# Performance work log

Hardware: AMD Instinct MI355X
Metric: run time of the kernel (lower is better)

Reference implementation:

```python
import jax, jax.numpy as jnp
import numpy as np

N, DIM, H, D, S, B = 30000, 256, 8, 64, 32, 8
INNER = H * D


def setup_inputs() -> dict:
    key = jax.random.key(0)
    ks = jax.random.split(key, 16)
    def w(k, shape, fan_in):
        return jax.random.normal(k, shape, dtype=jnp.float32) / np.sqrt(fan_in)
    x = jax.random.normal(ks[0], (N, DIM), dtype=jnp.float32)
    batch = jnp.sort(jax.random.randint(ks[1], (N,), 0, B))
    return {
        'x': x,
        'batch': batch,
        'W_fx': w(ks[2], (DIM, INNER), DIM), 'b_fx': jnp.zeros((INNER,), jnp.float32),
        'W_x': w(ks[3], (DIM, INNER), DIM), 'b_x': jnp.zeros((INNER,), jnp.float32),
        'W_slice': w(ks[4], (D, S), D), 'b_slice': jnp.zeros((S,), jnp.float32),
        'graph_temp': 0.5 * jnp.ones((1, H, 1), jnp.float32),
        'W_q': w(ks[5], (D, D), D), 'W_k': w(ks[6], (D, D), D), 'W_v': w(ks[7], (D, D), D),
        'W_out': w(ks[8], (INNER, DIM), INNER), 'b_out': jnp.zeros((DIM,), jnp.float32),
    }


def reference(x, batch, W_fx, b_fx, W_x, b_x, W_slice, b_slice, graph_temp,
              W_q, W_k, W_v, W_out, b_out):
    n = x.shape[0]
    scale = D ** -0.5
    fx = (x @ W_fx + b_fx).reshape(n, H, D)   # [N,H,D]
    xm = (x @ W_x + b_x).reshape(n, H, D)     # [N,H,D]
    # per-node slice assignment weights, tempered softmax over slices
    logits = (jnp.einsum('nhd,ds->nhs', xm, W_slice) + b_slice) / graph_temp
    w = jax.nn.softmax(logits, axis=-1)       # [N,H,S]
    onehot = jax.nn.one_hot(batch, B, dtype=x.dtype)  # [N,B]
    # scatter-add pooling per graph: slice_norm[b,h,s], slice_token[b,h,s,d]
    slice_norm = jax.ops.segment_sum(w, batch, num_segments=B)  # [B,H,S]
    wb = w[:, None, :, :] * onehot[:, :, None, None]            # [N,B,H,S]
    slice_token = jnp.einsum('nbhs,nhd->bhsd', wb, fx)
    slice_token = slice_token / (slice_norm[..., None] + 1e-5)
    # small attention over slice tokens
    q = jnp.einsum('bhsd,de->bhse', slice_token, W_q)
    k = jnp.einsum('bhsd,de->bhse', slice_token, W_k)
    v = jnp.einsum('bhsd,de->bhse', slice_token, W_v)
    attn = jax.nn.softmax(jnp.einsum('bhsd,bhtd->bhst', q, k) * scale, axis=-1)
    out_tok = jnp.einsum('bhst,bhtd->bhsd', attn, v)            # [B,H,S,D]
    # gather back to nodes with weighted reduction over slices
    tmp = jnp.einsum('nhs,bhsd->nbhd', w, out_tok)              # [N,B,H,D]
    out_x = jnp.einsum('nb,nbhd->nhd', onehot, tmp).reshape(n, INNER)
    return out_x @ W_out + b_out
```

## Files before the change

kernel.cpp:

```cpp
#include <hip/hip_runtime.h>

#define NDIM 256
#define INNER 512
#define NH 8
#define ND 64
#define NS 32
#define NB 8
#define NP 30208

typedef __attribute__((ext_vector_type(8))) short short8;
typedef __attribute__((ext_vector_type(4))) float f32x4;

static __device__ __forceinline__ short f2bf(float f) {
  unsigned u = __float_as_uint(f);
  unsigned r = (u + 0x7fffu + ((u >> 16) & 1u)) >> 16;
  return (short)r;
}
static __device__ __forceinline__ float bf2f(short s) {
  return __uint_as_float(((unsigned)(unsigned short)s) << 16);
}

static __device__ __forceinline__ void gl_lds16(const void* g, void* l) {
  __builtin_amdgcn_global_load_lds(
      (const __attribute__((address_space(1))) unsigned int*)g,
      (__attribute__((address_space(3))) unsigned int*)l, 16, 0, 0);
}

__global__ __launch_bounds__(256) void k_xsplit(
    const float* __restrict__ x, short* __restrict__ Xh, short* __restrict__ Xl,
    int total4)
{
  int id = blockIdx.x * 256 + threadIdx.x;
  if (id >= total4) return;
  float4 v = *(const float4*)&x[(size_t)id * 4];
  short h0 = f2bf(v.x), h1 = f2bf(v.y), h2 = f2bf(v.z), h3 = f2bf(v.w);
  short4 hv = make_short4(h0, h1, h2, h3);
  short4 lv = make_short4(f2bf(v.x - bf2f(h0)), f2bf(v.y - bf2f(h1)),
                          f2bf(v.z - bf2f(h2)), f2bf(v.w - bf2f(h3)));
  *(short4*)&Xh[(size_t)id * 4] = hv;
  *(short4*)&Xl[(size_t)id * 4] = lv;
}

__global__ __launch_bounds__(256) void k_prep(
    const float* __restrict__ Wfx, const float* __restrict__ Wx,
    const float* __restrict__ bx, const float* __restrict__ Wsl,
    const float* __restrict__ bsl,
    short* __restrict__ Bt1h, short* __restrict__ Bt1l,
    float* __restrict__ bcomb, int* __restrict__ seg)
{
  int id = blockIdx.x * 256 + threadIdx.x;
  if (id < 131072) {
    int k = id >> 9, n = id & 511;
    float v = Wfx[k * 512 + n];
    short hi = f2bf(v); short lo = f2bf(v - bf2f(hi));
    Bt1h[n * 256 + k] = hi; Bt1l[n * 256 + k] = lo;
  } else if (id < 196608) {
    int e = id - 131072;
    int c = e & 255, k = e >> 8;
    int h = c >> 5, s = c & 31;
    float acc = 0.f;
    #pragma unroll 8
    for (int d = 0; d < 64; d++) acc += Wx[k * 512 + h * 64 + d] * Wsl[d * 32 + s];
    short hi = f2bf(acc); short lo = f2bf(acc - bf2f(hi));
    Bt1h[(512 + c) * 256 + k] = hi; Bt1l[(512 + c) * 256 + k] = lo;
  } else if (id < 196864) {
    int c = id - 196608;
    int h = c >> 5, s = c & 31;
    float acc = bsl[s];
    #pragma unroll 8
    for (int d = 0; d < 64; d++) acc += bx[h * 64 + d] * Wsl[d * 32 + s];
    bcomb[c] = acc;
  } else if (id < 196880) {
    int v = id - 196864;
    seg[v] = (v == 0) ? 0 : 0x7fffffff;
  }
}

__global__ __launch_bounds__(256) void k_segs(
    const int* __restrict__ batch, int* __restrict__ seg, int N)
{
  int i = blockIdx.x * 256 + threadIdx.x;
  if (i >= N) return;
  int b = batch[i];
  int p = (i == 0) ? -1 : batch[i - 1];
  for (int v = p + 1; v <= b; v++)
    if (v >= 1) atomicMin(&seg[v], i);
  if (i == N - 1)
    for (int v = b + 1; v <= 8; v++) atomicMin(&seg[v], N);
}

__global__ __launch_bounds__(512, 4) void k_fxw(
    const short* __restrict__ Xh, const short* __restrict__ Xl,
    const short* __restrict__ Bt1h, const short* __restrict__ Bt1l,
    const float* __restrict__ bfx, const float* __restrict__ bcomb,
    const float* __restrict__ gtemp,
    short* __restrict__ fxTh, short* __restrict__ fxTl,
    short* __restrict__ wh_out, short* __restrict__ wl_out,
    int N, int ntiles)
{
  __shared__ __align__(16) short smem[32768];

  const int lid = blockIdx.x;
  const int xcd = lid & 7;
  const int idx = lid >> 3;
  const int ct  = idx % 6;
  const int rowt = xcd + 8 * (idx / 6);
  if (rowt >= ntiles) return;
  const int row0 = rowt * 128;
  const int tid = threadIdx.x;
  const int lane = tid & 63, l15 = lane & 15, quad = lane >> 4;
  const int wvi = tid >> 6;
  const int wm = wvi & 1, wn = wvi >> 1;
  const int ctbase = ct * 128;
  const int srow = lane & 15, schunk = lane >> 4;

  f32x4 acc[4][2];
  #pragma unroll
  for (int i = 0; i < 4; i++)
    #pragma unroll
    for (int j = 0; j < 2; j++) acc[i][j] = (f32x4){0.f, 0.f, 0.f, 0.f};

  int gr = row0 + wvi * 16 + srow;
  if (gr > N - 1) gr = N - 1;
  const int br = ctbase + wvi * 16 + srow;
  const size_t abase = (size_t)gr * 256 + schunk * 8;
  const size_t bbase = (size_t)br * 256 + schunk * 8;

#define STAGE(p, kt_) do {                                         \
    short* base_ = &smem[(p) * 16384];                             \
    gl_lds16(Xh + abase + (kt_) * 32, base_ + wvi * 512);          \
    gl_lds16(Xl + abase + (kt_) * 32, base_ + 4096 + wvi * 512);   \
    gl_lds16(Bt1h + bbase + (kt_) * 32, base_ + 8192 + wvi * 512); \
    gl_lds16(Bt1l + bbase + (kt_) * 32, base_ + 12288 + wvi * 512);\
  } while (0)

  STAGE(0, 0);

  #pragma unroll
  for (int kt = 0; kt < 8; kt++) {
    if (kt < 7) {
      STAGE((kt + 1) & 1, kt + 1);
      asm volatile("s_waitcnt vmcnt(4)" ::: "memory");
    } else {
      asm volatile("s_waitcnt vmcnt(0)" ::: "memory");
    }
    __builtin_amdgcn_s_barrier();
    asm volatile("" ::: "memory");

    const short* AhL = &smem[(kt & 1) * 16384];
    const short* AlL = AhL + 4096;
    const short* BhL = AhL + 8192;
    const short* BlL = AhL + 12288;

    short8 ah[4], al[4];
    #pragma unroll
    for (int mt = 0; mt < 4; mt++) {
      int rg = wm * 4 + mt;
      ah[mt] = *(const short8*)&AhL[rg * 512 + quad * 128 + l15 * 8];
      al[mt] = *(const short8*)&AlL[rg * 512 + quad * 128 + l15 * 8];
    }
    #pragma unroll
    for (int nt = 0; nt < 2; nt++) {
      int rg = wn * 2 + nt;
      short8 bh = *(const short8*)&BhL[rg * 512 + quad * 128 + l15 * 8];
      short8 bl = *(const short8*)&BlL[rg * 512 + quad * 128 + l15 * 8];
      #pragma unroll
      for (int mt = 0; mt < 4; mt++) {
        acc[mt][nt] = __builtin_amdgcn_mfma_f32_16x16x32_bf16(ah[mt], bh, acc[mt][nt], 0, 0, 0);
        acc[mt][nt] = __builtin_amdgcn_mfma_f32_16x16x32_bf16(ah[mt], bl, acc[mt][nt], 0, 0, 0);
        acc[mt][nt] = __builtin_amdgcn_mfma_f32_16x16x32_bf16(al[mt], bh, acc[mt][nt], 0, 0, 0);
      }
    }

    asm volatile("s_waitcnt lgkmcnt(0)" ::: "memory");
    __builtin_amdgcn_s_barrier();
  }
#undef STAGE

  if (ct < 4) {
    short (*T)[136] = (short(*)[136])&smem[0];
    #pragma unroll
    for (int pass = 0; pass < 2; pass++) {
      __syncthreads();
      #pragma unroll
      for (int nt = 0; nt < 2; nt++) {
        int cl = wn * 32 + nt * 16 + l15;
        float bias = bfx[ctbase + cl];
        #pragma unroll
        for (int mt = 0; mt < 4; mt++)
          #pragma unroll
          for (int r = 0; r < 4; r++) {
            int rl = wm * 64 + mt * 16 + quad * 4 + r;
            float v = acc[mt][nt][r] + bias;
            short hi2 = f2bf(v);
            T[cl][rl] = pass ? f2bf(v - bf2f(hi2)) : hi2;
          }
      }
      __syncthreads();
      short* dst = pass ? fxTl : fxTh;
      #pragma unroll
      for (int t = 0; t < 4; t++) {
        int idx2 = tid + t * 512;
        int row = idx2 >> 4, kc = (idx2 & 15) * 8;
        *(int4*)&dst[(size_t)(ctbase + row) * NP + row0 + kc] = *(const int4*)&T[row][kc];
      }
    }
  } else {
    int ct2 = ct - 4;
    int lcbase = ct2 * 128 + wn * 32;
    int h = lcbase >> 5;
    float inv_t = 1.0f / gtemp[h];
    int lc0 = lcbase + l15, lc1 = lcbase + 16 + l15;
    float b0 = bcomb[lc0], b1 = bcomb[lc1];
    #pragma unroll
    for (int mt = 0; mt < 4; mt++) {
      #pragma unroll
      for (int r = 0; r < 4; r++) {
        float s0 = (acc[mt][0][r] + b0) * inv_t;
        float s1 = (acc[mt][1][r] + b1) * inv_t;
        float m = fmaxf(s0, s1);
        #pragma unroll
        for (int off = 1; off < 16; off <<= 1) m = fmaxf(m, __shfl_xor(m, off, 16));
        float e0 = __expf(s0 - m), e1 = __expf(s1 - m);
        float sum = e0 + e1;
        #pragma unroll
        for (int off = 1; off < 16; off <<= 1) sum += __shfl_xor(sum, off, 16);
        float inv = 1.0f / sum;
        int row = row0 + wm * 64 + mt * 16 + quad * 4 + r;
        if (row < N) {
          float w0v = e0 * inv, w1v = e1 * inv;
          size_t base = (size_t)row * (NH * NS);
          short h0 = f2bf(w0v), h1 = f2bf(w1v);
          wh_out[base + lc0] = h0; wl_out[base + lc0] = f2bf(w0v - bf2f(h0));
          wh_out[base + lc1] = h1; wl_out[base + lc1] = f2bf(w1v - bf2f(h1));
        }
      }
    }
  }
}

__global__ __launch_bounds__(256) void k_scat(
    const short* __restrict__ wh, const short* __restrict__ wl,
    const short* __restrict__ fxTh, const short* __restrict__ fxTl,
    const int* __restrict__ seg,
    float* __restrict__ stok, float* __restrict__ snorm, int N)
{
  __shared__ short wth[32][136];
  __shared__ short wtl[32][136];
  __shared__ __align__(16) short fh[64][128];
  __shared__ __align__(16) short fl[64][128];
  __shared__ float ln[32];

  const int h = blockIdx.y;
  const int n0 = blockIdx.x * 512;
  const int tid = threadIdx.x;
  const int lane = tid & 63, l15 = lane & 15, quad = lane >> 4;
  const int wv = tid >> 6;
  const int nend = min(n0 + 512, N);
  const int lr4 = lane >> 4, lc16 = lane & 15;

  f32x4 acc0 = (f32x4){0.f, 0.f, 0.f, 0.f};
  f32x4 acc1 = (f32x4){0.f, 0.f, 0.f, 0.f};

  for (int b = 0; b < NB; b++) {
    int lo = max(seg[b], n0), hi = min(seg[b + 1], nend);
    if (lo >= hi) continue;
    if (tid < 32) ln[tid] = 0.f;
    int c0lo = (lo - n0) & ~127;
    int c0hi = hi - n0;
    for (int c0 = c0lo; c0 < c0hi; c0 += 128) {
      __syncthreads();

      #pragma unroll
      for (int t = 0; t < 4; t++) {
        int i = wv * 4 + t;
        int row = i * 4 + lr4;
        int cs = lc16 ^ (row & 7);
        size_t src = (size_t)(h * 64 + row) * NP + n0 + c0 + cs * 8;
        gl_lds16(fxTh + src, &fh[i * 4][0]);
        gl_lds16(fxTl + src, &fl[i * 4][0]);
      }

      #pragma unroll
      for (int t = 0; t < 2; t++) {
        int idx2 = tid + t * 256;
        int row = idx2 >> 2;
        int sc  = (idx2 & 3) * 8;
        int ng = n0 + c0 + row;
        short8 vh = (short8){0,0,0,0,0,0,0,0};
        short8 vl = (short8){0,0,0,0,0,0,0,0};
        if (ng >= lo && ng < hi) {
          size_t src = (size_t)ng * 256 + h * 32 + sc;
          vh = *(const short8*)&wh[src];
          vl = *(const short8*)&wl[src];
        }
        #pragma unroll
        for (int j = 0; j < 8; j++) {
          wth[sc + j][row] = vh[j];
          wtl[sc + j][row] = vl[j];
        }
      }
      __syncthreads();

      {
        int s = tid >> 3, g = tid & 7;
        float sum = 0.f;
        #pragma unroll
        for (int i2 = 0; i2 < 16; i2++) {
          int nl = g * 16 + i2;
          sum += bf2f(wth[s][nl]) + bf2f(wtl[s][nl]);
        }
        atomicAdd(&ln[s], sum);
      }

      for (int k0 = 0; k0 < 128; k0 += 32) {
        int gbase = n0 + c0 + k0;
        if (gbase + 32 <= lo || gbase >= hi) continue;
        short8 a0h = *(const short8*)&wth[l15][k0 + quad * 8];
        short8 a0l = *(const short8*)&wtl[l15][k0 + quad * 8];
        short8 a1h = *(const short8*)&wth[16 + l15][k0 + quad * 8];
        short8 a1l = *(const short8*)&wtl[16 + l15][k0 + quad * 8];
        int rB = wv * 16 + l15;
        int cB = ((k0 >> 3) + quad) ^ (rB & 7);
        short8 bh = *(const short8*)&fh[rB][cB * 8];
        short8 bl = *(const short8*)&fl[rB][cB * 8];
        acc0 = __builtin_amdgcn_mfma_f32_16x16x32_bf16(a0h, bh, acc0, 0, 0, 0);
        acc0 = __builtin_amdgcn_mfma_f32_16x16x32_bf16(a0h, bl, acc0, 0, 0, 0);
        acc0 = __builtin_amdgcn_mfma_f32_16x16x32_bf16(a0l, bh, acc0, 0, 0, 0);
        acc1 = __builtin_amdgcn_mfma_f32_16x16x32_bf16(a1h, bh, acc1, 0, 0, 0);
        acc1 = __builtin_amdgcn_mfma_f32_16x16x32_bf16(a1h, bl, acc1, 0, 0, 0);
        acc1 = __builtin_amdgcn_mfma_f32_16x16x32_bf16(a1l, bh, acc1, 0, 0, 0);
      }
    }
    __syncthreads();
    size_t base = ((size_t)b * NH + h) * NS;
    #pragma unroll
    for (int r = 0; r < 4; r++) {
      atomicAdd(&stok[(base + quad * 4 + r) * ND + wv * 16 + l15], acc0[r]);
      atomicAdd(&stok[(base + 16 + quad * 4 + r) * ND + wv * 16 + l15], acc1[r]);
    }
    if (tid < 32) atomicAdd(&snorm[base + tid], ln[tid]);
    acc0 = (f32x4){0.f, 0.f, 0.f, 0.f};
    acc1 = (f32x4){0.f, 0.f, 0.f, 0.f};
    __syncthreads();
  }
}

__global__ __launch_bounds__(256) void k_attn(
    const float* __restrict__ stok, const float* __restrict__ snorm,
    const float* __restrict__ Wq, const float* __restrict__ Wk,
    const float* __restrict__ Wv, const float* __restrict__ Wout,
    short* __restrict__ PTh, short* __restrict__ PTl)
{
  __shared__ __align__(16) float st[32][68];
  __shared__ __align__(16) float qs[32][68];
  __shared__ __align__(16) float ks[32][68];
  __shared__ __align__(16) float vs[32][68];
  __shared__ __align__(16) float at[32][36];
  __shared__ __align__(16) float ot[32][68];
  __shared__ __align__(16) float wo[64][256];

  const int bh = blockIdx.x;
  const int b = bh >> 3, h = bh & 7;
  const int tid = threadIdx.x;
  const int lane = tid & 63;
  const int wv = tid >> 6;

  {
    const float* wsrc = Wout + (size_t)h * 16384;
    float* wdst = &wo[0][0];
    #pragma unroll
    for (int r = 0; r < 16; r++) {
      int off = r * 1024 + wv * 256;
      gl_lds16(wsrc + off + lane * 4, wdst + off);
    }
  }

  for (int i = tid; i < 2048; i += 256) {
    int ss = i >> 6, dd = i & 63;
    float nrm = snorm[(size_t)bh * NS + ss] + 1e-5f;
    st[ss][dd] = stok[(size_t)bh * 2048 + i] / nrm;
  }
  __syncthreads();

  {
    float aq[8], ak[8], av[8];
    #pragma unroll
    for (int i = 0; i < 8; i++) { aq[i] = 0.f; ak[i] = 0.f; av[i] = 0.f; }
    for (int ch = 0; ch < 16; ch++) {
      float4 sv[8];
      #pragma unroll
      for (int i = 0; i < 8; i++) sv[i] = *(const float4*)&st[wv * 8 + i][ch * 4];
      #pragma unroll
      for (int d = 0; d < 4; d++) {
        int dd = ch * 4 + d;
        float wq = Wq[dd * 64 + lane];
        float wk = Wk[dd * 64 + lane];
        float wvv = Wv[dd * 64 + lane];
        #pragma unroll
        for (int i = 0; i < 8; i++) {
          float sd = (d == 0) ? sv[i].x : (d == 1) ? sv[i].y : (d == 2) ? sv[i].z : sv[i].w;
          aq[i] = fmaf(sd, wq, aq[i]);
          ak[i] = fmaf(sd, wk, ak[i]);
          av[i] = fmaf(sd, wvv, av[i]);
        }
      }
    }
    #pragma unroll
    for (int i = 0; i < 8; i++) {
      qs[wv * 8 + i][lane] = aq[i];
      ks[wv * 8 + i][lane] = ak[i];
      vs[wv * 8 + i][lane] = av[i];
    }
  }
  __syncthreads();

  {
    const int si = tid >> 3, tj0 = (tid & 7) * 4;
    float a0 = 0.f, a1 = 0.f, a2 = 0.f, a3 = 0.f;
    for (int ch = 0; ch < 16; ch++) {
      float4 q4 = *(const float4*)&qs[si][ch * 4];
      float4 k0 = *(const float4*)&ks[tj0 + 0][ch * 4];
      float4 k1 = *(const float4*)&ks[tj0 + 1][ch * 4];
      float4 k2 = *(const float4*)&ks[tj0 + 2][ch * 4];
      float4 k3 = *(const float4*)&ks[tj0 + 3][ch * 4];
      a0 += q4.x * k0.x + q4.y * k0.y + q4.z * k0.z + q4.w * k0.w;
      a1 += q4.x * k1.x + q4.y * k1.y + q4.z * k1.z + q4.w * k1.w;
      a2 += q4.x * k2.x + q4.y * k2.y + q4.z * k2.z + q4.w * k2.w;
// ... 209 lines not shown
          *(int4*)&Ah[row][kc] = vh;
          *(int4*)&Al[row][kc] = vl;
        }
        #pragma unroll
        for (int t = 0; t < 2; t++) {
          int i = tid + t * 256;
          int row = i >> 2, kc = (i & 3) * 8;
          size_t src = ((size_t)b * NDIM + ctbase + row) * 256 + kt * 32 + kc;
          *(int4*)&Bh[row][kc] = *(const int4*)&PTh[src];
          *(int4*)&Bl[row][kc] = *(const int4*)&PTl[src];
        }
        __syncthreads();

        short8 ah[4], al[4];
        #pragma unroll
        for (int mt = 0; mt < 4; mt++) {
          int m = wm * 64 + mt * 16 + l15;
          ah[mt] = *(const short8*)&Ah[m][quad * 8];
          al[mt] = *(const short8*)&Al[m][quad * 8];
        }
        #pragma unroll
        for (int nt = 0; nt < 4; nt++) {
          int n = wn * 64 + nt * 16 + l15;
          short8 bh = *(const short8*)&Bh[n][quad * 8];
          short8 bl = *(const short8*)&Bl[n][quad * 8];
          #pragma unroll
          for (int mt = 0; mt < 4; mt++) {
            acc[mt][nt] = __builtin_amdgcn_mfma_f32_16x16x32_bf16(ah[mt], bh, acc[mt][nt], 0, 0, 0);
            acc[mt][nt] = __builtin_amdgcn_mfma_f32_16x16x32_bf16(ah[mt], bl, acc[mt][nt], 0, 0, 0);
            acc[mt][nt] = __builtin_amdgcn_mfma_f32_16x16x32_bf16(al[mt], bh, acc[mt][nt], 0, 0, 0);
          }
        }
        __syncthreads();
      }
      i0 = j;
    }
  }

  #pragma unroll
  for (int nt = 0; nt < 4; nt++) {
    int c = ctbase + wn * 64 + nt * 16 + l15;
    float bias = bout[c];
    #pragma unroll
    for (int mt = 0; mt < 4; mt++)
      #pragma unroll
      for (int r = 0; r < 4; r++) {
        int row = row0 + wm * 64 + mt * 16 + quad * 4 + r;
        if (row < N) out[(size_t)row * NDIM + c] = acc[mt][nt][r] + bias;
      }
  }
}

extern "C" void kernel_launch(void* const* d_in, const int* in_sizes, int n_in,
                              void* d_out, int out_size, void* d_ws, size_t ws_size,
                              hipStream_t stream) {
  const float* x      = (const float*)d_in[0];
  const int*   batch  = (const int*)d_in[1];
  const float* Wfx    = (const float*)d_in[2];
  const float* bfx    = (const float*)d_in[3];
  const float* Wx     = (const float*)d_in[4];
  const float* bx     = (const float*)d_in[5];
  const float* Wsl    = (const float*)d_in[6];
  const float* bsl    = (const float*)d_in[7];
  const float* gtemp  = (const float*)d_in[8];
  const float* Wq     = (const float*)d_in[9];
  const float* Wk     = (const float*)d_in[10];
  const float* Wv     = (const float*)d_in[11];
  const float* Wout   = (const float*)d_in[12];
  const float* bout   = (const float*)d_in[13];
  float* out = (float*)d_out;

  const int N = in_sizes[0] / NDIM;

  float* stok  = (float*)d_ws;
  float* snorm = stok + 131072;
  float* bcomb = snorm + 2048;
  int*   seg   = (int*)(bcomb + 256);
  short* Bt1h  = (short*)(seg + 16);
  short* Bt1l  = Bt1h + 196608;
  short* Xh    = Bt1l + 196608;
  short* Xl    = Xh + 7680000;
  short* whb   = Xl + 7680000;
  short* wlb   = whb + (size_t)NP * 256;
  short* fxTh  = wlb + (size_t)NP * 256;
  short* fxTl  = fxTh + (size_t)512 * NP;
  short* PTh   = fxTl + (size_t)512 * NP;
  short* PTl   = PTh + 524288;

  hipMemsetAsync(stok, 0, (size_t)(131072 + 2048) * sizeof(float), stream);

  k_xsplit<<<(N * 64 + 255) / 256, 256, 0, stream>>>(x, Xh, Xl, N * 64);

  k_prep<<<770, 256, 0, stream>>>(Wfx, Wx, bx, Wsl, bsl, Bt1h, Bt1l, bcomb, seg);

  k_segs<<<(N + 255) / 256, 256, 0, stream>>>(batch, seg, N);

  const int ntiles = (N + 127) / 128;
  const int qmax = (ntiles + 7) / 8;
  k_fxw<<<8 * qmax * 6, 512, 0, stream>>>(Xh, Xl, Bt1h, Bt1l, bfx, bcomb, gtemp,
                                          fxTh, fxTl, whb, wlb, N, ntiles);

  dim3 g2((N + 511) / 512, NH);
  k_scat<<<g2, 256, 0, stream>>>(whb, wlb, fxTh, fxTl, seg, stok, snorm, N);

  k_attn<<<NB * NH, 256, 0, stream>>>(stok, snorm, Wq, Wk, Wv, Wout, PTh, PTl);

  dim3 g5(2, (N + 127) / 128);
  k_outw<<<g5, 256, 0, stream>>>(whb, wlb, PTh, PTl, batch, bout, out, N);
}
```

Baseline: 268.9 us.

## Keep X row tile resident in LDS and loop over all column tiles per block

```diff
diff --git a/kernel.cpp b/kernel.cpp
--- a/kernel.cpp
+++ b/kernel.cpp
@@ -89,7 +89,7 @@
     for (int v = b + 1; v <= 8; v++) atomicMin(&seg[v], N);
 }
 
-__global__ __launch_bounds__(512, 4) void k_fxw(
+__global__ __launch_bounds__(512) void k_fxw(
     const short* __restrict__ Xh, const short* __restrict__ Xl,
     const short* __restrict__ Bt1h, const short* __restrict__ Bt1l,
     const float* __restrict__ bfx, const float* __restrict__ bcomb,
@@ -98,145 +98,155 @@
     short* __restrict__ wh_out, short* __restrict__ wl_out,
     int N, int ntiles)
 {
-  __shared__ __align__(16) short smem[32768];
-
-  const int lid = blockIdx.x;
-  const int xcd = lid & 7;
-  const int idx = lid >> 3;
-  const int ct  = idx % 6;
-  const int rowt = xcd + 8 * (idx / 6);
+  __shared__ __align__(16) short smem[81920];
+
+  const int rowt = blockIdx.x;
   if (rowt >= ntiles) return;
   const int row0 = rowt * 128;
   const int tid = threadIdx.x;
   const int lane = tid & 63, l15 = lane & 15, quad = lane >> 4;
   const int wvi = tid >> 6;
   const int wm = wvi & 1, wn = wvi >> 1;
-  const int ctbase = ct * 128;
   const int srow = lane & 15, schunk = lane >> 4;
 
-  f32x4 acc[4][2];
-  #pragma unroll
-  for (int i = 0; i < 4; i++)
-    #pragma unroll
-    for (int j = 0; j < 2; j++) acc[i][j] = (f32x4){0.f, 0.f, 0.f, 0.f};
+  short* XhL = &smem[0];
+  short* XlL = &smem[32768];
 
   int gr = row0 + wvi * 16 + srow;
   if (gr > N - 1) gr = N - 1;
-  const int br = ctbase + wvi * 16 + srow;
-  const size_t abase = (size_t)gr * 256 + schunk * 8;
-  const size_t bbase = (size_t)br * 256 + schunk * 8;
-
-#define STAGE(p, kt_) do {                                         \
-    short* base_ = &smem[(p) * 16384];                             \
-    gl_lds16(Xh + abase + (kt_) * 32, base_ + wvi * 512);          \
-    gl_lds16(Xl + abase + (kt_) * 32, base_ + 4096 + wvi * 512);   \
-    gl_lds16(Bt1h + bbase + (kt_) * 32, base_ + 8192 + wvi * 512); \
-    gl_lds16(Bt1l + bbase + (kt_) * 32, base_ + 12288 + wvi * 512);\
-  } while (0)
-
-  STAGE(0, 0);
-
+  const size_t xbase = (size_t)gr * 256 + schunk * 8;
   #pragma unroll
   for (int kt = 0; kt < 8; kt++) {
-    if (kt < 7) {
-      STAGE((kt + 1) & 1, kt + 1);
-      asm volatile("s_waitcnt vmcnt(4)" ::: "memory");
+    gl_lds16(Xh + xbase + kt * 32, XhL + kt * 4096 + wvi * 512);
+    gl_lds16(Xl + xbase + kt * 32, XlL + kt * 4096 + wvi * 512);
+  }
+
+  const size_t bthr = (size_t)(wvi * 16 + srow) * 256 + schunk * 8;
+
+#define STAGE_B(p, ct_, kt_) do {                                          \
+    short* bb_ = &smem[65536 + (p) * 8192];                                \
+    size_t s_ = bthr + (size_t)(ct_) * 32768 + (kt_) * 32;                 \
+    gl_lds16(Bt1h + s_, bb_ + wvi * 512);                                  \
+    gl_lds16(Bt1l + s_, bb_ + 4096 + wvi * 512);                           \
+  } while (0)
+
+  STAGE_B(0, 0, 0);
+
+  for (int ct = 0; ct < 6; ++ct) {
+    if (ct > 0) STAGE_B(0, ct, 0);
+
+    f32x4 acc[4][2];
+    #pragma unroll
+    for (int i = 0; i < 4; i++)
+      #pragma unroll
+      for (int j = 0; j < 2; j++) acc[i][j] = (f32x4){0.f, 0.f, 0.f, 0.f};
+
+    #pragma unroll
+    for (int kt = 0; kt < 8; kt++) {
+      if (kt < 7) {
+        STAGE_B((kt + 1) & 1, ct, kt + 1);
+        asm volatile("s_waitcnt vmcnt(2)" ::: "memory");
+      } else {
+        asm volatile("s_waitcnt vmcnt(0)" ::: "memory");
+      }
+      __builtin_amdgcn_s_barrier();
+      asm volatile("" ::: "memory");
+
+      const short* BhL = &smem[65536 + (kt & 1) * 8192];
+      const short* BlL = BhL + 4096;
+
+      short8 ah[4], al[4];
+      #pragma unroll
+      for (int mt = 0; mt < 4; mt++) {
+        int off = kt * 4096 + (wm * 4 + mt) * 512 + quad * 128 + l15 * 8;
+        ah[mt] = *(const short8*)&XhL[off];
+        al[mt] = *(const short8*)&XlL[off];
+      }
+      #pragma unroll
+      for (int nt = 0; nt < 2; nt++) {
+        int rg = wn * 2 + nt;
+        short8 bh = *(const short8*)&BhL[rg * 512 + quad * 128 + l15 * 8];
+        short8 bl = *(const short8*)&BlL[rg * 512 + quad * 128 + l15 * 8];
+        #pragma unroll
+        for (int mt = 0; mt < 4; mt++) {
+          acc[mt][nt] = __builtin_amdgcn_mfma_f32_16x16x32_bf16(ah[mt], bh, acc[mt][nt], 0, 0, 0);
+          acc[mt][nt] = __builtin_amdgcn_mfma_f32_16x16x32_bf16(ah[mt], bl, acc[mt][nt], 0, 0, 0);
+          acc[mt][nt] = __builtin_amdgcn_mfma_f32_16x16x32_bf16(al[mt], bh, acc[mt][nt], 0, 0, 0);
+        }
+      }
+
+      asm volatile("s_waitcnt lgkmcnt(0)" ::: "memory");
+      __builtin_amdgcn_s_barrier();
+    }
+
+    if (ct < 4) {
+      short (*T)[136] = (short(*)[136])&smem[65536];
+      const int ctbase = ct * 128;
+      for (int h2 = 0; h2 < 2; h2++) {
+        #pragma unroll
+        for (int pass = 0; pass < 2; pass++) {
+          if ((wn >> 1) == h2) {
+            int cl = (wn & 1) * 32;
+            #pragma unroll
+            for (int nt = 0; nt < 2; nt++) {
+              int c = cl + nt * 16 + l15;
+              float bias = bfx[ctbase + h2 * 64 + c];
+              #pragma unroll
+              for (int mt = 0; mt < 4; mt++)
+                #pragma unroll
+                for (int r = 0; r < 4; r++) {
+                  int rl = wm * 64 + mt * 16 + quad * 4 + r;
+                  float v = acc[mt][nt][r] + bias;
+                  short hi2 = f2bf(v);
+                  T[c][rl] = pass ? f2bf(v - bf2f(hi2)) : hi2;
+                }
+            }
+          }
+          __syncthreads();
+          short* dst = pass ? fxTl : fxTh;
+          #pragma unroll
+          for (int t = 0; t < 2; t++) {
+            int idx2 = tid + t * 512;
+            int c = idx2 >> 4, ch = (idx2 & 15) * 8;
+            *(int4*)&dst[(size_t)(ctbase + h2 * 64 + c) * NP + row0 + ch] =
+                *(const int4*)&T[c][ch];
+          }
+          __syncthreads();
+        }
+      }
     } else {
-      asm volatile("s_waitcnt vmcnt(0)" ::: "memory");
-    }
-    __builtin_amdgcn_s_barrier();
-    asm volatile("" ::: "memory");
-
-    const short* AhL = &smem[(kt & 1) * 16384];
-    const short* AlL = AhL + 4096;
-    const short* BhL = AhL + 8192;
-    const short* BlL = AhL + 12288;
-
-    short8 ah[4], al[4];
-    #pragma unroll
-    for (int mt = 0; mt < 4; mt++) {
-      int rg = wm * 4 + mt;
-      ah[mt] = *(const short8*)&AhL[rg * 512 + quad * 128 + l15 * 8];
-      al[mt] = *(const short8*)&AlL[rg * 512 + quad * 128 + l15 * 8];
-    }
-    #pragma unroll
-    for (int nt = 0; nt < 2; nt++) {
-      int rg = wn * 2 + nt;
-      short8 bh = *(const short8*)&BhL[rg * 512 + quad * 128 + l15 * 8];
-      short8 bl = *(const short8*)&BlL[rg * 512 + quad * 128 + l15 * 8];
+      int lcbase = (ct - 4) * 128 + wn * 32;
+      int h = lcbase >> 5;
+      float inv_t = 1.0f / gtemp[h];
+      int lc0 = lcbase + l15, lc1 = lcbase + 16 + l15;
+      float b0 = bcomb[lc0], b1 = bcomb[lc1];
       #pragma unroll
       for (int mt = 0; mt < 4; mt++) {
-        acc[mt][nt] = __builtin_amdgcn_mfma_f32_16x16x32_bf16(ah[mt], bh, acc[mt][nt], 0, 0, 0);
-        acc[mt][nt] = __builtin_amdgcn_mfma_f32_16x16x32_bf16(ah[mt], bl, acc[mt][nt], 0, 0, 0);
-        acc[mt][nt] = __builtin_amdgcn_mfma_f32_16x16x32_bf16(al[mt], bh, acc[mt][nt], 0, 0, 0);
-      }
-    }
-
-    asm volatile("s_waitcnt lgkmcnt(0)" ::: "memory");
-    __builtin_amdgcn_s_barrier();
-  }
-#undef STAGE
-
-  if (ct < 4) {
-    short (*T)[136] = (short(*)[136])&smem[0];
-    #pragma unroll
-    for (int pass = 0; pass < 2; pass++) {
-      __syncthreads();
-      #pragma unroll
-      for (int nt = 0; nt < 2; nt++) {
-        int cl = wn * 32 + nt * 16 + l15;
-        float bias = bfx[ctbase + cl];
-        #pragma unroll
-        for (int mt = 0; mt < 4; mt++)
+        #pragma unroll
+        for (int r = 0; r < 4; r++) {
+          float s0 = (acc[mt][0][r] + b0) * inv_t;
+          float s1 = (acc[mt][1][r] + b1) * inv_t;
+          float m = fmaxf(s0, s1);
           #pragma unroll
-          for (int r = 0; r < 4; r++) {
-            int rl = wm * 64 + mt * 16 + quad * 4 + r;
-            float v = acc[mt][nt][r] + bias;
-            short hi2 = f2bf(v);
-            T[cl][rl] = pass ? f2bf(v - bf2f(hi2)) : hi2;
+          for (int off = 1; off < 16; off <<= 1) m = fmaxf(m, __shfl_xor(m, off, 16));
+          float e0 = __expf(s0 - m), e1 = __expf(s1 - m);
+          float sum = e0 + e1;
+          #pragma unroll
+          for (int off = 1; off < 16; off <<= 1) sum += __shfl_xor(sum, off, 16);
+          float inv = 1.0f / sum;
+          int row = row0 + wm * 64 + mt * 16 + quad * 4 + r;
+          if (row < N) {
+            float w0v = e0 * inv, w1v = e1 * inv;
+            size_t base = (size_t)row * (NH * NS);
+            short h0 = f2bf(w0v), h1 = f2bf(w1v);
+            wh_out[base + lc0] = h0; wl_out[base + lc0] = f2bf(w0v - bf2f(h0));
+            wh_out[base + lc1] = h1; wl_out[base + lc1] = f2bf(w1v - bf2f(h1));
           }
-      }
-      __syncthreads();
-      short* dst = pass ? fxTl : fxTh;
-      #pragma unroll
-      for (int t = 0; t < 4; t++) {
-        int idx2 = tid + t * 512;
-        int row = idx2 >> 4, kc = (idx2 & 15) * 8;
-        *(int4*)&dst[(size_t)(ctbase + row) * NP + row0 + kc] = *(const int4*)&T[row][kc];
-      }
-    }
-  } else {
-    int ct2 = ct - 4;
-    int lcbase = ct2 * 128 + wn * 32;
-    int h = lcbase >> 5;
-    float inv_t = 1.0f / gtemp[h];
-    int lc0 = lcbase + l15, lc1 = lcbase + 16 + l15;
-    float b0 = bcomb[lc0], b1 = bcomb[lc1];
-    #pragma unroll
-    for (int mt = 0; mt < 4; mt++) {
-      #pragma unroll
-      for (int r = 0; r < 4; r++) {
-        float s0 = (acc[mt][0][r] + b0) * inv_t;
-        float s1 = (acc[mt][1][r] + b1) * inv_t;
-        float m = fmaxf(s0, s1);
-        #pragma unroll
-        for (int off = 1; off < 16; off <<= 1) m = fmaxf(m, __shfl_xor(m, off, 16));
-        float e0 = __expf(s0 - m), e1 = __expf(s1 - m);
-        float sum = e0 + e1;
-        #pragma unroll
-        for (int off = 1; off < 16; off <<= 1) sum += __shfl_xor(sum, off, 16);
-        float inv = 1.0f / sum;
-        int row = row0 + wm * 64 + mt * 16 + quad * 4 + r;
-        if (row < N) {
-          float w0v = e0 * inv, w1v = e1 * inv;
-          size_t base = (size_t)row * (NH * NS);
-          short h0 = f2bf(w0v), h1 = f2bf(w1v);
-          wh_out[base + lc0] = h0; wl_out[base + lc0] = f2bf(w0v - bf2f(h0));
-          wh_out[base + lc1] = h1; wl_out[base + lc1] = f2bf(w1v - bf2f(h1));
-        }
-      }
-    }
-  }
+        }
+      }
+    }
+  }
+#undef STAGE_B
 }
 
 __global__ __launch_bounds__(256) void k_scat(
@@ -733,9 +743,8 @@
   k_segs<<<(N + 255) / 256, 256, 0, stream>>>(batch, seg, N);
 
   const int ntiles = (N + 127) / 128;
-  const int qmax = (ntiles + 7) / 8;
-  k_fxw<<<8 * qmax * 6, 512, 0, stream>>>(Xh, Xl, Bt1h, Bt1l, bfx, bcomb, gtemp,
-                                          fxTh, fxTl, whb, wlb, N, ntiles);
+  k_fxw<<<ntiles, 512, 0, stream>>>(Xh, Xl, Bt1h, Bt1l, bfx, bcomb, gtemp,
+                                    fxTh, fxTl, whb, wlb, N, ntiles);
 
   dim3 g2((N + 511) / 512, NH);
   k_scat<<<g2, 256, 0, stream>>>(whb, wlb, fxTh, fxTl, seg, stok, snorm, N);
```

Result: no change. 268.4 us (-0.2%).

## Fuse scatter pooling into projection GEMM kernel, dropping fx round trip

Applied to the files above, without the earlier changes.

```diff
diff --git a/kernel.cpp b/kernel.cpp
--- a/kernel.cpp
+++ b/kernel.cpp
@@ -89,261 +89,263 @@
     for (int v = b + 1; v <= 8; v++) atomicMin(&seg[v], N);
 }
 
-__global__ __launch_bounds__(512, 4) void k_fxw(
+__global__ __launch_bounds__(512) void k_fxw(
     const short* __restrict__ Xh, const short* __restrict__ Xl,
     const short* __restrict__ Bt1h, const short* __restrict__ Bt1l,
     const float* __restrict__ bfx, const float* __restrict__ bcomb,
-    const float* __restrict__ gtemp,
-    short* __restrict__ fxTh, short* __restrict__ fxTl,
+    const float* __restrict__ gtemp, const int* __restrict__ seg,
     short* __restrict__ wh_out, short* __restrict__ wl_out,
+    float* __restrict__ stok, float* __restrict__ snorm,
     int N, int ntiles)
 {
-  __shared__ __align__(16) short smem[32768];
-
-  const int lid = blockIdx.x;
-  const int xcd = lid & 7;
-  const int idx = lid >> 3;
-  const int ct  = idx % 6;
-  const int rowt = xcd + 8 * (idx / 6);
+  __shared__ __align__(16) short smem[67584];
+  const int WT = 32768;
+  const int FXL = 50176;
+
+  const int rowt = blockIdx.x;
   if (rowt >= ntiles) return;
   const int row0 = rowt * 128;
   const int tid = threadIdx.x;
   const int lane = tid & 63, l15 = lane & 15, quad = lane >> 4;
   const int wvi = tid >> 6;
   const int wm = wvi & 1, wn = wvi >> 1;
-  const int ctbase = ct * 128;
   const int srow = lane & 15, schunk = lane >> 4;
 
-  f32x4 acc[4][2];
+  int segr[9];
   #pragma unroll
-  for (int i = 0; i < 4; i++)
-    #pragma unroll
-    for (int j = 0; j < 2; j++) acc[i][j] = (f32x4){0.f, 0.f, 0.f, 0.f};
+  for (int i = 0; i < 9; i++) segr[i] = seg[i];
+  const int tileHi = min(row0 + 128, N);
+  int nact = 0, bUni = 0;
+  #pragma unroll
+  for (int b = 0; b < 8; b++) {
+    int lo = max(segr[b], row0), hi = min(segr[b + 1], tileHi);
+    if (lo < hi) { nact++; bUni = b; }
+  }
+  const bool uniform = (nact == 1) && (tileHi - row0 == 128);
 
   int gr = row0 + wvi * 16 + srow;
   if (gr > N - 1) gr = N - 1;
-  const int br = ctbase + wvi * 16 + srow;
   const size_t abase = (size_t)gr * 256 + schunk * 8;
-  const size_t bbase = (size_t)br * 256 + schunk * 8;
-
-#define STAGE(p, kt_) do {                                         \
-    short* base_ = &smem[(p) * 16384];                             \
-    gl_lds16(Xh + abase + (kt_) * 32, base_ + wvi * 512);          \
-    gl_lds16(Xl + abase + (kt_) * 32, base_ + 4096 + wvi * 512);   \
-    gl_lds16(Bt1h + bbase + (kt_) * 32, base_ + 8192 + wvi * 512); \
-    gl_lds16(Bt1l + bbase + (kt_) * 32, base_ + 12288 + wvi * 512);\
+  const size_t bthr = (size_t)(wvi * 16 + srow) * 256 + schunk * 8;
+
+#define STAGE(p, ct_, kt_) do {                                                  \
+    short* base_ = &smem[(p) * 16384];                                           \
+    gl_lds16(Xh + abase + (kt_) * 32, base_ + wvi * 512);                        \
+    gl_lds16(Xl + abase + (kt_) * 32, base_ + 4096 + wvi * 512);                 \
+    gl_lds16(Bt1h + bthr + (size_t)(ct_) * 32768 + (kt_) * 32, base_ + 8192 + wvi * 512);  \
+    gl_lds16(Bt1l + bthr + (size_t)(ct_) * 32768 + (kt_) * 32, base_ + 12288 + wvi * 512); \
   } while (0)
 
-  STAGE(0, 0);
-
+  unsigned wsH[16], wsL[16];
   #pragma unroll
-  for (int kt = 0; kt < 8; kt++) {
-    if (kt < 7) {
-      STAGE((kt + 1) & 1, kt + 1);
-      asm volatile("s_waitcnt vmcnt(4)" ::: "memory");
+  for (int i = 0; i < 16; i++) { wsH[i] = 0; wsL[i] = 0; }
+
+  STAGE(0, 4, 0);
+
+  for (int pi = 0; pi < 6; pi++) {
+    const int ct = (pi == 0) ? 4 : (pi == 3) ? 5 : (pi < 3 ? pi - 1 : pi - 2);
+
+    f32x4 acc[4][2];
+    #pragma unroll
+    for (int i = 0; i < 4; i++)
+      #pragma unroll
+      for (int j = 0; j < 2; j++) acc[i][j] = (f32x4){0.f, 0.f, 0.f, 0.f};
+
+    #pragma unroll
+    for (int kt = 0; kt < 8; kt++) {
+      if (kt < 7) {
+        STAGE((kt + 1) & 1, ct, kt + 1);
+        asm volatile("s_waitcnt vmcnt(4)" ::: "memory");
+      } else {
+        asm volatile("s_waitcnt vmcnt(0)" ::: "memory");
+      }
+      __builtin_amdgcn_s_barrier();
+      asm volatile("" ::: "memory");
+
+      const short* AhL = &smem[(kt & 1) * 16384];
+      const short* AlL = AhL + 4096;
+      const short* BhL = AhL + 8192;
+      const short* BlL = AhL + 12288;
+
+      short8 ah[4], al[4];
+      #pragma unroll
+      for (int mt = 0; mt < 4; mt++) {
+        int rg = wm * 4 + mt;
+        ah[mt] = *(const short8*)&AhL[rg * 512 + quad * 128 + l15 * 8];
+        al[mt] = *(const short8*)&AlL[rg * 512 + quad * 128 + l15 * 8];
+      }
+      #pragma unroll
+      for (int nt = 0; nt < 2; nt++) {
+        int rg = wn * 2 + nt;
+        short8 bh = *(const short8*)&BhL[rg * 512 + quad * 128 + l15 * 8];
+        short8 bl = *(const short8*)&BlL[rg * 512 + quad * 128 + l15 * 8];
+        #pragma unroll
+        for (int mt = 0; mt < 4; mt++) {
+          acc[mt][nt] = __builtin_amdgcn_mfma_f32_16x16x32_bf16(ah[mt], bh, acc[mt][nt], 0, 0, 0);
+          acc[mt][nt] = __builtin_amdgcn_mfma_f32_16x16x32_bf16(ah[mt], bl, acc[mt][nt], 0, 0, 0);
+          acc[mt][nt] = __builtin_amdgcn_mfma_f32_16x16x32_bf16(al[mt], bh, acc[mt][nt], 0, 0, 0);
+        }
+      }
+
+      asm volatile("s_waitcnt lgkmcnt(0)" ::: "memory");
+      __builtin_amdgcn_s_barrier();
+    }
+
+    if (pi < 5) {
+      const int nct = (pi + 1 == 3) ? 5 : (pi + 1 < 3 ? pi : pi - 1);
+      STAGE(0, nct, 0);
+    }
+
+    if (ct >= 4) {
+      const int h = (ct - 4) * 4 + wn;
+      const float inv_t = 1.0f / gtemp[h];
+      const int lcb = (ct - 4) * 128 + wn * 32;
+      const int lc0 = lcb + l15, lc1 = lcb + 16 + l15;
+      const float b0 = bcomb[lc0], b1 = bcomb[lc1];
+      float snp0 = 0.f, snp1 = 0.f;
+      #pragma unroll
+      for (int mt = 0; mt < 4; mt++) {
+        #pragma unroll
+        for (int r = 0; r < 4; r++) {
+          float s0 = (acc[mt][0][r] + b0) * inv_t;
+          float s1 = (acc[mt][1][r] + b1) * inv_t;
+          float m = fmaxf(s0, s1);
+          #pragma unroll
+          for (int off = 1; off < 16; off <<= 1) m = fmaxf(m, __shfl_xor(m, off, 16));
+          float e0 = __expf(s0 - m), e1 = __expf(s1 - m);
+          float sum = e0 + e1;
+          #pragma unroll
+          for (int off = 1; off < 16; off <<= 1) sum += __shfl_xor(sum, off, 16);
+          float inv = 1.0f / sum;
+          float w0v = e0 * inv, w1v = e1 * inv;
+          int rl = wm * 64 + mt * 16 + quad * 4 + r;
+          int row = row0 + rl;
+          short h0 = f2bf(w0v); short l0 = f2bf(w0v - bf2f(h0));
+          short h1 = f2bf(w1v); short l1 = f2bf(w1v - bf2f(h1));
+          if (row < N) {
+            size_t base = (size_t)row * 256;
+            wh_out[base + lc0] = h0; wl_out[base + lc0] = l0;
+            wh_out[base + lc1] = h1; wl_out[base + lc1] = l1;
+          }
+          if (wn < 2) {
+            smem[WT + wn * 4352 + l15 * 136 + rl] = h0;
+            smem[WT + (2 + wn) * 4352 + l15 * 136 + rl] = l0;
+            smem[WT + wn * 4352 + (16 + l15) * 136 + rl] = h1;
+            smem[WT + (2 + wn) * 4352 + (16 + l15) * 136 + rl] = l1;
+          } else {
+            wsH[mt * 4 + r] = (unsigned)(unsigned short)h0 | ((unsigned)(unsigned short)h1 << 16);
+            wsL[mt * 4 + r] = (unsigned)(unsigned short)l0 | ((unsigned)(unsigned short)l1 << 16);
+          }
+          if (uniform) {
+            snp0 += w0v; snp1 += w1v;
+          } else if (row < tileHi) {
+            int be = 0;
+            #pragma unroll
+            for (int k = 1; k <= 8; k++) be += (segr[k] <= row) ? 1 : 0;
+            atomicAdd(&snorm[(be * NH + h) * NS + l15], w0v);
+            atomicAdd(&snorm[(be * NH + h) * NS + 16 + l15], w1v);
+          }
+        }
+      }
+      if (uniform) {
+        atomicAdd(&snorm[(bUni * NH + h) * NS + l15], snp0);
+        atomicAdd(&snorm[(bUni * NH + h) * NS + 16 + l15], snp1);
+      }
+      asm volatile("s_waitcnt lgkmcnt(0)" ::: "memory");
+      __builtin_amdgcn_s_barrier();
     } else {
-      asm volatile("s_waitcnt vmcnt(0)" ::: "memory");
-    }
-    __builtin_amdgcn_s_barrier();
-    asm volatile("" ::: "memory");
-
-    const short* AhL = &smem[(kt & 1) * 16384];
-    const short* AlL = AhL + 4096;
-    const short* BhL = AhL + 8192;
-    const short* BlL = AhL + 12288;
-
-    short8 ah[4], al[4];
-    #pragma unroll
-    for (int mt = 0; mt < 4; mt++) {
-      int rg = wm * 4 + mt;
-      ah[mt] = *(const short8*)&AhL[rg * 512 + quad * 128 + l15 * 8];
-      al[mt] = *(const short8*)&AlL[rg * 512 + quad * 128 + l15 * 8];
-    }
-    #pragma unroll
-    for (int nt = 0; nt < 2; nt++) {
-      int rg = wn * 2 + nt;
-      short8 bh = *(const short8*)&BhL[rg * 512 + quad * 128 + l15 * 8];
-      short8 bl = *(const short8*)&BlL[rg * 512 + quad * 128 + l15 * 8];
-      #pragma unroll
-      for (int mt = 0; mt < 4; mt++) {
-        acc[mt][nt] = __builtin_amdgcn_mfma_f32_16x16x32_bf16(ah[mt], bh, acc[mt][nt], 0, 0, 0);
-        acc[mt][nt] = __builtin_amdgcn_mfma_f32_16x16x32_bf16(ah[mt], bl, acc[mt][nt], 0, 0, 0);
-        acc[mt][nt] = __builtin_amdgcn_mfma_f32_16x16x32_bf16(al[mt], bh, acc[mt][nt], 0, 0, 0);
-      }
-    }
-
-    asm volatile("s_waitcnt lgkmcnt(0)" ::: "memory");
-    __builtin_amdgcn_s_barrier();
-  }
-#undef STAGE
-
-  if (ct < 4) {
-    short (*T)[136] = (short(*)[136])&smem[0];
-    #pragma unroll
-    for (int pass = 0; pass < 2; pass++) {
-      __syncthreads();
-      #pragma unroll
-      for (int nt = 0; nt < 2; nt++) {
-        int cl = wn * 32 + nt * 16 + l15;
-        float bias = bfx[ctbase + cl];
+      if ((ct & 1) && wvi >= 4) {
+        int slot = wn - 2;
         #pragma unroll
         for (int mt = 0; mt < 4; mt++)
           #pragma unroll
           for (int r = 0; r < 4; r++) {
             int rl = wm * 64 + mt * 16 + quad * 4 + r;
-            float v = acc[mt][nt][r] + bias;
-            short hi2 = f2bf(v);
-            T[cl][rl] = pass ? f2bf(v - bf2f(hi2)) : hi2;
-          }
-      }
-      __syncthreads();
-      short* dst = pass ? fxTl : fxTh;
-      #pragma unroll
-      for (int t = 0; t < 4; t++) {
-        int idx2 = tid + t * 512;
-        int row = idx2 >> 4, kc = (idx2 & 15) * 8;
-        *(int4*)&dst[(size_t)(ctbase + row) * NP + row0 + kc] = *(const int4*)&T[row][kc];
-      }
-    }
-  } else {
-    int ct2 = ct - 4;
-    int lcbase = ct2 * 128 + wn * 32;
-    int h = lcbase >> 5;
-    float inv_t = 1.0f / gtemp[h];
-    int lc0 = lcbase + l15, lc1 = lcbase + 16 + l15;
-    float b0 = bcomb[lc0], b1 = bcomb[lc1];
-    #pragma unroll
-    for (int mt = 0; mt < 4; mt++) {
-      #pragma unroll
-      for (int r = 0; r < 4; r++) {
-        float s0 = (acc[mt][0][r] + b0) * inv_t;
-        float s1 = (acc[mt][1][r] + b1) * inv_t;
-        float m = fmaxf(s0, s1);
-        #pragma unroll
-        for (int off = 1; off < 16; off <<= 1) m = fmaxf(m, __shfl_xor(m, off, 16));
-        float e0 = __expf(s0 - m), e1 = __expf(s1 - m);
-        float sum = e0 + e1;
-        #pragma unroll
-        for (int off = 1; off < 16; off <<= 1) sum += __shfl_xor(sum, off, 16);
-        float inv = 1.0f / sum;
-        int row = row0 + wm * 64 + mt * 16 + quad * 4 + r;
-        if (row < N) {
-          float w0v = e0 * inv, w1v = e1 * inv;
-          size_t base = (size_t)row * (NH * NS);
-          short h0 = f2bf(w0v), h1 = f2bf(w1v);
-          wh_out[base + lc0] = h0; wl_out[base + lc0] = f2bf(w0v - bf2f(h0));
-          wh_out[base + lc1] = h1; wl_out[base + lc1] = f2bf(w1v - bf2f(h1));
-        }
-      }
-    }
-  }
-}
-
-__global__ __launch_bounds__(256) void k_scat(
-    const short* __restrict__ wh, const short* __restrict__ wl,
-    const short* __restrict__ fxTh, const short* __restrict__ fxTl,
-    const int* __restrict__ seg,
-    float* __restrict__ stok, float* __restrict__ snorm, int N)
-{
-  __shared__ short wth[32][136];
-  __shared__ short wtl[32][136];
-  __shared__ __align__(16) short fh[64][128];
-  __shared__ __align__(16) short fl[64][128];
-  __shared__ float ln[32];
-
-  const int h = blockIdx.y;
-  const int n0 = blockIdx.x * 512;
-  const int tid = threadIdx.x;
-  const int lane = tid & 63, l15 = lane & 15, quad = lane >> 4;
-  const int wv = tid >> 6;
-  const int nend = min(n0 + 512, N);
-  const int lr4 = lane >> 4, lc16 = lane & 15;
-
-  f32x4 acc0 = (f32x4){0.f, 0.f, 0.f, 0.f};
-  f32x4 acc1 = (f32x4){0.f, 0.f, 0.f, 0.f};
-
-  for (int b = 0; b < NB; b++) {
-    int lo = max(seg[b], n0), hi = min(seg[b + 1], nend);
-    if (lo >= hi) continue;
-    if (tid < 32) ln[tid] = 0.f;
-    int c0lo = (lo - n0) & ~127;
-    int c0hi = hi - n0;
-    for (int c0 = c0lo; c0 < c0hi; c0 += 128) {
-      __syncthreads();
-
-      #pragma unroll
-      for (int t = 0; t < 4; t++) {
-        int i = wv * 4 + t;
-        int row = i * 4 + lr4;
-        int cs = lc16 ^ (row & 7);
-        size_t src = (size_t)(h * 64 + row) * NP + n0 + c0 + cs * 8;
-        gl_lds16(fxTh + src, &fh[i * 4][0]);
-        gl_lds16(fxTl + src, &fl[i * 4][0]);
-      }
-
-      #pragma unroll
-      for (int t = 0; t < 2; t++) {
-        int idx2 = tid + t * 256;
-        int row = idx2 >> 2;
-        int sc  = (idx2 & 3) * 8;
-        int ng = n0 + c0 + row;
-        short8 vh = (short8){0,0,0,0,0,0,0,0};
-        short8 vl = (short8){0,0,0,0,0,0,0,0};
-        if (ng >= lo && ng < hi) {
-          size_t src = (size_t)ng * 256 + h * 32 + sc;
-          vh = *(const short8*)&wh[src];
-          vl = *(const short8*)&wl[src];
-        }
-        #pragma unroll
-        for (int j = 0; j < 8; j++) {
-          wth[sc + j][row] = vh[j];
-          wtl[sc + j][row] = vl[j];
-        }
-      }
-      __syncthreads();
-
-      {
-        int s = tid >> 3, g = tid & 7;
-        float sum = 0.f;
-        #pragma unroll
-        for (int i2 = 0; i2 < 16; i2++) {
-          int nl = g * 16 + i2;
-          sum += bf2f(wth[s][nl]) + bf2f(wtl[s][nl]);
-        }
-        atomicAdd(&ln[s], sum);
-      }
-
-      for (int k0 = 0; k0 < 128; k0 += 32) {
-        int gbase = n0 + c0 + k0;
-        if (gbase + 32 <= lo || gbase >= hi) continue;
-        short8 a0h = *(const short8*)&wth[l15][k0 + quad * 8];
-        short8 a0l = *(const short8*)&wtl[l15][k0 + quad * 8];
-        short8 a1h = *(const short8*)&wth[16 + l15][k0 + quad * 8];
-        short8 a1l = *(const short8*)&wtl[16 + l15][k0 + quad * 8];
-        int rB = wv * 16 + l15;
-        int cB = ((k0 >> 3) + quad) ^ (rB & 7);
-        short8 bh = *(const short8*)&fh[rB][cB * 8];
-        short8 bl = *(const short8*)&fl[rB][cB * 8];
-        acc0 = __builtin_amdgcn_mfma_f32_16x16x32_bf16(a0h, bh, acc0, 0, 0, 0);
-        acc0 = __builtin_amdgcn_mfma_f32_16x16x32_bf16(a0h, bl, acc0, 0, 0, 0);
-        acc0 = __builtin_amdgcn_mfma_f32_16x16x32_bf16(a0l, bh, acc0, 0, 0, 0);
-        acc1 = __builtin_amdgcn_mfma_f32_16x16x32_bf16(a1h, bh, acc1, 0, 0, 0);
-        acc1 = __builtin_amdgcn_mfma_f32_16x16x32_bf16(a1h, bl, acc1, 0, 0, 0);
-        acc1 = __builtin_amdgcn_mfma_f32_16x16x32_bf16(a1l, bh, acc1, 0, 0, 0);
-      }
-    }
-    __syncthreads();
-    size_t base = ((size_t)b * NH + h) * NS;
-    #pragma unroll
-    for (int r = 0; r < 4; r++) {
-      atomicAdd(&stok[(base + quad * 4 + r) * ND + wv * 16 + l15], acc0[r]);
-      atomicAdd(&stok[(base + 16 + quad * 4 + r) * ND + wv * 16 + l15], acc1[r]);
-    }
-    if (tid < 32) atomicAdd(&snorm[base + tid], ln[tid]);
-    acc0 = (f32x4){0.f, 0.f, 0.f, 0.f};
-    acc1 = (f32x4){0.f, 0.f, 0.f, 0.f};
-    __syncthreads();
-  }
+            unsigned ph = wsH[mt * 4 + r], pl = wsL[mt * 4 + r];
+            smem[WT + slot * 4352 + l15 * 136 + rl] = (short)(ph & 0xffff);
+            smem[WT + (2 + slot) * 4352 + l15 * 136 + rl] = (short)(pl & 0xffff);
+            smem[WT + slot * 4352 + (16 + l15) * 136 + rl] = (short)(ph >> 16);
+            smem[WT + (2 + slot) * 4352 + (16 + l15) * 136 + rl] = (short)(pl >> 16);
+          }
+      }
+
+      const int sb = wvi & 1, db = wvi >> 1;
+      #pragma unroll
+      for (int hh = 0; hh < 2; hh++) {
+        const int h = ct * 2 + hh;
+        if ((wn >> 1) == hh) {
+          int cw = wn & 1;
+          #pragma unroll
+          for (int nt = 0; nt < 2; nt++) {
+            int d = cw * 32 + nt * 16 + l15;
+            float bias = bfx[ct * 128 + hh * 64 + d];
+            #pragma unroll
+            for (int mt = 0; mt < 4; mt++)
+              #pragma unroll
+              for (int r = 0; r < 4; r++) {
+                int rl = wm * 64 + mt * 16 + quad * 4 + r;
+                float v = acc[mt][nt][r] + bias;
+                short hi2 = f2bf(v);
+                smem[FXL + d * 136 + rl] = hi2;
+                smem[FXL + 8704 + d * 136 + rl] = f2bf(v - bf2f(hi2));
+              }
+          }
+        }
+        asm volatile("s_waitcnt lgkmcnt(0)" ::: "memory");
+        __builtin_amdgcn_s_barrier();
+
+        if (uniform) {
+          f32x4 as = (f32x4){0.f, 0.f, 0.f, 0.f};
+          #pragma unroll
+          for (int kk = 0; kk < 4; kk++) {
+            short8 aH = *(const short8*)&smem[WT + hh * 4352 + (sb * 16 + l15) * 136 + kk * 32 + quad * 8];
+            short8 aL = *(const short8*)&smem[WT + (2 + hh) * 4352 + (sb * 16 + l15) * 136 + kk * 32 + quad * 8];
+            short8 bH = *(const short8*)&smem[FXL + (db * 16 + l15) * 136 + kk * 32 + quad * 8];
+            short8 bL = *(const short8*)&smem[FXL + 8704 + (db * 16 + l15) * 136 + kk * 32 + quad * 8];
+            as = __builtin_amdgcn_mfma_f32_16x16x32_bf16(aH, bH, as, 0, 0, 0);
+            as = __builtin_amdgcn_mfma_f32_16x16x32_bf16(aH, bL, as, 0, 0, 0);
+            as = __builtin_amdgcn_mfma_f32_16x16x32_bf16(aL, bH, as, 0, 0, 0);
+          }
+          size_t base = ((size_t)bUni * NH + h) * NS;
+          #pragma unroll
+          for (int r = 0; r < 4; r++)
+            atomicAdd(&stok[(base + sb * 16 + quad * 4 + r) * ND + db * 16 + l15], as[r]);
+        } else {
+          #pragma unroll
+          for (int b = 0; b < 8; b++) {
+            int lo = max(segr[b], row0), hi = min(segr[b + 1], tileHi);
+            if (lo >= hi) continue;
+            f32x4 as = (f32x4){0.f, 0.f, 0.f, 0.f};
+            #pragma unroll
+            for (int kk = 0; kk < 4; kk++) {
+              int nc0 = row0 + kk * 32;
+              if (nc0 + 32 <= lo || nc0 >= hi) continue;
+              short8 aH = *(const short8*)&smem[WT + hh * 4352 + (sb * 16 + l15) * 136 + kk * 32 + quad * 8];
+              short8 aL = *(const short8*)&smem[WT + (2 + hh) * 4352 + (sb * 16 + l15) * 136 + kk * 32 + quad * 8];
+              short8 bH = *(const short8*)&smem[FXL + (db * 16 + l15) * 136 + kk * 32 + quad * 8];
+              short8 bL = *(const short8*)&smem[FXL + 8704 + (db * 16 + l15) * 136 + kk * 32 + quad * 8];
+              int nb = nc0 + quad * 8;
+              #pragma unroll
+              for (int j = 0; j < 8; j++) {
+                int rw = nb + j;
+                if (rw < lo || rw >= hi) { aH[j] = 0; aL[j] = 0; }
+              }
+              as = __builtin_amdgcn_mfma_f32_16x16x32_bf16(aH, bH, as, 0, 0, 0);
+              as = __builtin_amdgcn_mfma_f32_16x16x32_bf16(aH, bL, as, 0, 0, 0);
+              as = __builtin_amdgcn_mfma_f32_16x16x32_bf16(aL, bH, as, 0, 0, 0);
+            }
+            size_t base = ((size_t)b * NH + h) * NS;
+            #pragma unroll
+            for (int r = 0; r < 4; r++)
+              atomicAdd(&stok[(base + sb * 16 + quad * 4 + r) * ND + db * 16 + l15], as[r]);
+          }
+        }
+        asm volatile("s_waitcnt lgkmcnt(0)" ::: "memory");
+        __builtin_amdgcn_s_barrier();
+      }
+    }
+  }
+#undef STAGE
 }
 
 __global__ __launch_bounds__(256) void k_attn(
@@ -719,9 +721,7 @@
   short* Xl    = Xh + 7680000;
   short* whb   = Xl + 7680000;
   short* wlb   = whb + (size_t)NP * 256;
-  short* fxTh  = wlb + (size_t)NP * 256;
-  short* fxTl  = fxTh + (size_t)512 * NP;
-  short* PTh   = fxTl + (size_t)512 * NP;
+  short* PTh   = wlb + (size_t)NP * 256;
   short* PTl   = PTh + 524288;
 
   hipMemsetAsync(stok, 0, (size_t)(131072 + 2048) * sizeof(float), stream);
@@ -733,12 +733,8 @@
   k_segs<<<(N + 255) / 256, 256, 0, stream>>>(batch, seg, N);
 
   const int ntiles = (N + 127) / 128;
-  const int qmax = (ntiles + 7) / 8;
-  k_fxw<<<8 * qmax * 6, 512, 0, stream>>>(Xh, Xl, Bt1h, Bt1l, bfx, bcomb, gtemp,
-                                          fxTh, fxTl, whb, wlb, N, ntiles);
-
-  dim3 g2((N + 511) / 512, NH);
-  k_scat<<<g2, 256, 0, stream>>>(whb, wlb, fxTh, fxTl, seg, stok, snorm, N);
+  k_fxw<<<ntiles, 512, 0, stream>>>(Xh, Xl, Bt1h, Bt1l, bfx, bcomb, gtemp, seg,
+                                    whb, wlb, stok, snorm, N, ntiles);
 
   k_attn<<<NB * NH, 256, 0, stream>>>(stok, snorm, Wq, Wk, Wv, Wout, PTh, PTl);
 
```

Result: slower. 350.6 us (+30.4%).
